# Kernel tuning notes

Hardware: AMD Instinct MI355X
Metric: run time of the kernel (lower is better)

The kernel has to match this reference:

```python
import jax, jax.numpy as jnp
import numpy as np

EPS = 1e-5
MIN_NORM = 1e-15


def artanh(x):
    return jnp.arctanh(jnp.clip(x, -1.0 + EPS, 1.0 - EPS))


def expmap0(u, c):
    # Poincare ball exponential map at the origin (HGCN style)
    sqrt_c = jnp.sqrt(c)
    u_norm = jnp.maximum(jnp.linalg.norm(u, axis=-1, keepdims=True), MIN_NORM)
    return jnp.tanh(sqrt_c * u_norm) * u / (sqrt_c * u_norm)


def mobius_add(x, y, c):
    x2 = jnp.sum(x * x, axis=-1, keepdims=True)
    y2 = jnp.sum(y * y, axis=-1, keepdims=True)
    xy = jnp.sum(x * y, axis=-1, keepdims=True)
    num = (1.0 + 2.0 * c * xy + c * y2) * x + (1.0 - c * x2) * y
    den = 1.0 + 2.0 * c * xy + (c ** 2) * x2 * y2
    return num / jnp.maximum(den, MIN_NORM)


def sqdist(x, y, c):
    sqrt_c = jnp.sqrt(c)
    ma = mobius_add(-x, y, c)
    dist = (2.0 / sqrt_c) * artanh(sqrt_c * jnp.linalg.norm(ma, axis=-1))
    return dist ** 2


def setup_inputs() -> dict:
    key = jax.random.key(0)
    k1, k2 = jax.random.split(key)
    B, T, N, C, K = 8, 12, 325, 32, 100
    # scale down so points land well inside the unit ball (curvature c=1)
    node_repr = 0.05 * jax.random.normal(k1, (B, T, N, C), dtype=jnp.float32)
    centroid_weight = 0.05 * jax.random.normal(k2, (K, C), dtype=jnp.float32)
    c = jnp.ones((1,), dtype=jnp.float32)
    return {"node_repr": node_repr, "centroid_weight": centroid_weight, "c": c}


def reference(node_repr, centroid_weight, c):
    cc = c[0]
    B, T, N, C = node_repr.shape
    # centroid embedding lookup of arange(K) == the weight table itself
    centroids = expmap0(centroid_weight, cc)          # [K, C]
    x = node_repr[..., None, :]                        # [B, T, N, 1, C]
    node_centroid_dist = sqdist(x, centroids, cc)      # [B, T, N, K] via broadcast
    graph_centroid_dist = jnp.sum(node_centroid_dist, axis=1) / N  # [B, N, K] (faithful to dim=1 in source)
    return graph_centroid_dist, node_centroid_dist
```

## Files before the change

kernel.cpp:

```cpp
#include <hip/hip_runtime.h>

namespace {
constexpr int B = 8, T = 12, N = 325, C = 32, K = 100;
constexpr int KPAD = 36;
constexpr int NPB = 5;
constexpr int NPAIRS = N / NPB;
constexpr float EPSF = 1e-5f;
constexpr float MIN_NORM = 1e-15f;
}

__global__ __launch_bounds__(512, 2) void hcd_kernel(
    const float* __restrict__ x_g,
    const float* __restrict__ cw,
    const float* __restrict__ cptr,
    float* __restrict__ out0,
    float* __restrict__ out1)
{
  __shared__ float yl[K][KPAD];
  __shared__ float y2l[K];
  __shared__ float xl[NPB][T][KPAD];
  __shared__ float x2l[NPB][T];

  const int tid = threadIdx.x;
  const int b  = blockIdx.x / NPAIRS;
  const int np = blockIdx.x % NPAIRS;
  const int n0 = np * NPB;
  const float c  = cptr[0];
  const float sc = sqrtf(c);
  const float inv_c4 = 4.f / c;
  const float HLN2 = 0.34657359028f;
  const float TLOG2E = 2.88539008178f;

  for (int idx = tid; idx < NPB * T * (C / 4); idx += 512) {
    int nl = idx / (T * (C / 4));
    int r  = idx - nl * (T * (C / 4));
    int t  = r >> 3;
    int q  = r & 7;
    int n  = n0 + nl;
    float4 v = *(const float4*)(x_g + ((((size_t)(b * T + t)) * N + n) * C + 4 * q));
    *(float4*)&xl[nl][t][4 * q] = v;
  }

  if (tid < K) {
    float u[C];
    float u2 = 0.f;
    #pragma unroll
    for (int q = 0; q < C / 4; ++q) {
      float4 v = *(const float4*)(cw + tid * C + 4 * q);
      u[4*q+0] = v.x; u[4*q+1] = v.y; u[4*q+2] = v.z; u[4*q+3] = v.w;
    }
    #pragma unroll
    for (int i = 0; i < C; ++i) u2 = fmaf(u[i], u[i], u2);
    float z = sc * fmaxf(sqrtf(u2), MIN_NORM);
    float E  = exp2f(z * TLOG2E);
    float th = (E - 1.f) * __builtin_amdgcn_rcpf(E + 1.f);
    float f  = th * __builtin_amdgcn_rcpf(z);
    #pragma unroll
    for (int q = 0; q < C / 4; ++q) {
      float4 v = make_float4(f*u[4*q+0], f*u[4*q+1], f*u[4*q+2], f*u[4*q+3]);
      *(float4*)&yl[tid][4 * q] = v;
    }
    y2l[tid] = f * f * u2;
  }
  __syncthreads();

  if (tid < NPB * T) {
    int nl = tid / T, t = tid - nl * T;
    float s = 0.f;
    #pragma unroll
    for (int i = 0; i < C; ++i) s = fmaf(xl[nl][t][i], xl[nl][t][i], s);
    x2l[nl][t] = s;
  }
  __syncthreads();

  const int grp = tid / K;
  const int k   = tid - grp * K;
  if (grp < NPB) {
    const int n = n0 + grp;

    float yk[C];
    #pragma unroll
    for (int q = 0; q < C / 4; ++q) {
      float4 v = *(const float4*)&yl[k][4 * q];
      yk[4*q+0] = v.x; yk[4*q+1] = v.y; yk[4*q+2] = v.z; yk[4*q+3] = v.w;
    }
    const float y2 = y2l[k];
    const float c2 = c * c;
    const float tc = 2.f * c;

    float d[T];
    #pragma unroll
    for (int t = 0; t < T; ++t) d[t] = 0.f;
    #pragma unroll
    for (int q = 0; q < C / 4; ++q) {
      #pragma unroll
      for (int t = 0; t < T; ++t) {
        float4 xv = *(const float4*)&xl[grp][t][4 * q];
        float acc = d[t];
        acc = fmaf(xv.x, yk[4*q+0], acc);
        acc = fmaf(xv.y, yk[4*q+1], acc);
        acc = fmaf(xv.z, yk[4*q+2], acc);
        acc = fmaf(xv.w, yk[4*q+3], acc);
        d[t] = acc;
      }
    }

    float ssum = 0.f;
    #pragma unroll
    for (int t = 0; t < T; ++t) {
      const float x2 = x2l[grp][t];
      const float xy = -d[t];
      const float A  = fmaf(tc, xy, 1.f) + c * y2;
      const float Bc = 1.f - c * x2;
      float num2 = A * A * x2 + Bc * Bc * y2 + 2.f * A * Bc * xy;
      num2 = fmaxf(num2, 0.f);
      float den = fmaf(c2 * x2, y2, fmaf(tc, xy, 1.f));
      den = fmaxf(den, MIN_NORM);
      float s_ = sc * __builtin_amdgcn_sqrtf(num2);
      s_ = fminf(s_, (1.f - EPSF) * den);
      float r  = (den + s_) * __builtin_amdgcn_rcpf(den - s_);
      float at = HLN2 * __builtin_amdgcn_logf(r);
      float d2 = inv_c4 * at * at;
      ssum += d2;
      out1[(((size_t)(b * T + t)) * N + n) * K + k] = d2;
    }
    out0[((size_t)b * N + n) * K + k] = ssum * (1.f / (float)N);
  }
}

extern "C" void kernel_launch(void* const* d_in, const int* in_sizes, int n_in,
                              void* d_out, int out_size, void* d_ws, size_t ws_size,
                              hipStream_t stream) {
  const void* xp = nullptr; const void* cwp = nullptr; const void* cp = nullptr;
  for (int i = 0; i < n_in; ++i) {
    if (in_sizes[i] == B * T * N * C)      xp  = d_in[i];
    else if (in_sizes[i] == K * C)         cwp = d_in[i];
    else if (in_sizes[i] == 1)             cp  = d_in[i];
  }
  if (!xp)  xp  = d_in[0];
  if (!cwp) cwp = d_in[1];
  if (!cp)  cp  = d_in[n_in - 1];

  float* out0 = (float*)d_out;
  float* out1 = out0 + (size_t)B * N * K;

  hipLaunchKernelGGL(hcd_kernel, dim3(B * NPAIRS), dim3(512), 0, stream,
                     (const float*)xp, (const float*)cwp, (const float*)cp,
                     out0, out1);
}
```

Before: 17.30 us.

## Read node rows directly from global memory with wave-uniform scalar loads, smaller blocks

Drops the shared-memory staging of node rows. Each 128-lane group now handles one node, and the dot product reads x from global memory through a readfirstlane-uniform base address, so the compiler can issue scalar loads. Blocks shrink to 256 threads covering 2 nodes, with padded lanes clamped, and the grid grows to about 163 blocks per batch. This removes one barrier and the LDS traffic, but every block recomputes the centroid expmap more often, and the scalar loads may add latency.

```diff
diff --git a/kernel.cpp b/kernel.cpp
--- a/kernel.cpp
+++ b/kernel.cpp
@@ -3,13 +3,13 @@
 namespace {
 constexpr int B = 8, T = 12, N = 325, C = 32, K = 100;
 constexpr int KPAD = 36;
-constexpr int NPB = 5;
-constexpr int NPAIRS = N / NPB;
+constexpr int NPB = 2;
+constexpr int NPAIRS = (N + NPB - 1) / NPB;
 constexpr float EPSF = 1e-5f;
 constexpr float MIN_NORM = 1e-15f;
 }
 
-__global__ __launch_bounds__(512, 2) void hcd_kernel(
+__global__ __launch_bounds__(256) void hcd_kernel(
     const float* __restrict__ x_g,
     const float* __restrict__ cw,
     const float* __restrict__ cptr,
@@ -18,7 +18,6 @@
 {
   __shared__ float yl[K][KPAD];
   __shared__ float y2l[K];
-  __shared__ float xl[NPB][T][KPAD];
   __shared__ float x2l[NPB][T];
 
   const int tid = threadIdx.x;
@@ -30,16 +29,6 @@
   const float inv_c4 = 4.f / c;
   const float HLN2 = 0.34657359028f;
   const float TLOG2E = 2.88539008178f;
-
-  for (int idx = tid; idx < NPB * T * (C / 4); idx += 512) {
-    int nl = idx / (T * (C / 4));
-    int r  = idx - nl * (T * (C / 4));
-    int t  = r >> 3;
-    int q  = r & 7;
-    int n  = n0 + nl;
-    float4 v = *(const float4*)(x_g + ((((size_t)(b * T + t)) * N + n) * C + 4 * q));
-    *(float4*)&xl[nl][t][4 * q] = v;
-  }
 
   if (tid < K) {
     float u[C];
@@ -62,54 +51,60 @@
     }
     y2l[tid] = f * f * u2;
   }
-  __syncthreads();
 
-  if (tid < NPB * T) {
-    int nl = tid / T, t = tid - nl * T;
-    float s = 0.f;
-    #pragma unroll
-    for (int i = 0; i < C; ++i) s = fmaf(xl[nl][t][i], xl[nl][t][i], s);
-    x2l[nl][t] = s;
+  if (tid >= 128 && tid < 128 + NPB * T) {
+    int i  = tid - 128;
+    int nl = i / T, t = i - nl * T;
+    int n  = n0 + nl;
+    if (n < N) {
+      const float* xr = x_g + ((size_t)(b * T + t) * N + n) * C;
+      float s = 0.f;
+      #pragma unroll
+      for (int q = 0; q < C / 4; ++q) {
+        float4 v = *(const float4*)(xr + 4 * q);
+        s = fmaf(v.x, v.x, s); s = fmaf(v.y, v.y, s);
+        s = fmaf(v.z, v.z, s); s = fmaf(v.w, v.w, s);
+      }
+      x2l[nl][t] = s;
+    }
   }
   __syncthreads();
 
-  const int grp = tid / K;
-  const int k   = tid - grp * K;
-  if (grp < NPB) {
-    const int n = n0 + grp;
+  const int grp = tid >> 7;
+  const int k   = tid & 127;
+  const int n   = n0 + grp;
+  if (n < N) {
+    const int kc = (k < K) ? k : (K - 1);
 
     float yk[C];
     #pragma unroll
     for (int q = 0; q < C / 4; ++q) {
-      float4 v = *(const float4*)&yl[k][4 * q];
+      float4 v = *(const float4*)&yl[kc][4 * q];
       yk[4*q+0] = v.x; yk[4*q+1] = v.y; yk[4*q+2] = v.z; yk[4*q+3] = v.w;
     }
-    const float y2 = y2l[k];
+    const float y2 = y2l[kc];
     const float c2 = c * c;
     const float tc = 2.f * c;
 
-    float d[T];
-    #pragma unroll
-    for (int t = 0; t < T; ++t) d[t] = 0.f;
-    #pragma unroll
-    for (int q = 0; q < C / 4; ++q) {
-      #pragma unroll
-      for (int t = 0; t < T; ++t) {
-        float4 xv = *(const float4*)&xl[grp][t][4 * q];
-        float acc = d[t];
-        acc = fmaf(xv.x, yk[4*q+0], acc);
-        acc = fmaf(xv.y, yk[4*q+1], acc);
-        acc = fmaf(xv.z, yk[4*q+2], acc);
-        acc = fmaf(xv.w, yk[4*q+3], acc);
-        d[t] = acc;
-      }
-    }
+    int rowbase = ((b * T) * N + n) * C;
+    rowbase = __builtin_amdgcn_readfirstlane(rowbase);
 
     float ssum = 0.f;
     #pragma unroll
     for (int t = 0; t < T; ++t) {
+      const float* xr = x_g + rowbase + t * (N * C);
+      float a0 = 0.f, a1 = 0.f, a2 = 0.f, a3 = 0.f;
+      #pragma unroll
+      for (int j = 0; j < C; j += 4) {
+        a0 = fmaf(xr[j+0], yk[j+0], a0);
+        a1 = fmaf(xr[j+1], yk[j+1], a1);
+        a2 = fmaf(xr[j+2], yk[j+2], a2);
+        a3 = fmaf(xr[j+3], yk[j+3], a3);
+      }
+      const float dot = (a0 + a1) + (a2 + a3);
+
       const float x2 = x2l[grp][t];
-      const float xy = -d[t];
+      const float xy = -dot;
       const float A  = fmaf(tc, xy, 1.f) + c * y2;
       const float Bc = 1.f - c * x2;
       float num2 = A * A * x2 + Bc * Bc * y2 + 2.f * A * Bc * xy;
@@ -122,9 +117,11 @@
       float at = HLN2 * __builtin_amdgcn_logf(r);
       float d2 = inv_c4 * at * at;
       ssum += d2;
-      out1[(((size_t)(b * T + t)) * N + n) * K + k] = d2;
+      if (k < K)
+        out1[(((size_t)(b * T + t)) * N + n) * K + k] = d2;
     }
-    out0[((size_t)b * N + n) * K + k] = ssum * (1.f / (float)N);
+    if (k < K)
+      out0[((size_t)b * N + n) * K + k] = ssum * (1.f / (float)N);
   }
 }
 
@@ -144,7 +141,7 @@
   float* out0 = (float*)d_out;
   float* out1 = out0 + (size_t)B * N * K;
 
-  hipLaunchKernelGGL(hcd_kernel, dim3(B * NPAIRS), dim3(512), 0, stream,
+  hipLaunchKernelGGL(hcd_kernel, dim3(B * NPAIRS), dim3(256), 0, stream,
                      (const float*)xp, (const float*)cwp, (const float*)cp,
                      out0, out1);
 }
```

New measurement: 18.65 us. 1.08x slower.
